# Optimization experiments

Measured on AMD Instinct MI355X. Metric: run time of the kernel, lower is better.

The kernel has to match this reference:

```python
import jax, jax.numpy as jnp
import numpy as np

MAX_VAL = 10000.0


def _erode(x, kernel):
    # x: (B, C, H, W); kernel: (kh, kw) flat structuring element (nonzero = active)
    kh, kw = kernel.shape
    oy, ox = kh // 2, kw // 2  # origin = center (rounding toward zero)
    padded = jnp.pad(
        x,
        ((0, 0), (0, 0), (oy, kh - oy - 1), (ox, kw - ox - 1)),
        mode="constant",
        constant_values=MAX_VAL,
    )
    # neighborhood bias: 0 where kernel != 0, -max_val where kernel == 0
    # output[p] = min_k ( padded[p + k] - neighborhood[k] )
    neigh = jnp.where(kernel == 0, -MAX_VAL, 0.0).astype(x.dtype)
    H, W = x.shape[-2], x.shape[-1]
    out = None
    for i in range(kh):  # small fixed k*k loop; no conv/im2col blow-up
        for j in range(kw):
            v = padded[:, :, i:i + H, j:j + W] - neigh[i, j]
            out = v if out is None else jnp.minimum(out, v)
    return out


def setup_inputs() -> dict:
    key = jax.random.key(0)
    x = jax.random.normal(key, (8, 8, 1024, 1024), dtype=jnp.float32)
    kernel = jnp.ones((3, 3), dtype=jnp.float32)
    return {"x": x, "kernel": kernel}


def reference(x, kernel):
    return _erode(x, kernel)
```

## Files before the change

kernel.cpp:

```cpp
#include <hip/hip_runtime.h>

#define MAXV 10000.0f

__global__ __launch_bounds__(256)
void erode3x3_kernel(const float* __restrict__ x,
                     const float* __restrict__ kern,
                     float* __restrict__ out,
                     int H, int W, int segs ) {
    long long idx = (long long)blockIdx.x * blockDim.x + threadIdx.x;
    int seg = (int)(idx % segs);
    int y   = (int)((idx / segs) % H);
    long long bc = idx / ((long long)segs * (long long)H);

    float nv[3][3];
#pragma unroll
    for (int i = 0; i < 3; ++i)
#pragma unroll
        for (int j = 0; j < 3; ++j)
            nv[i][j] = (kern[i * 3 + j] == 0.0f) ? -MAXV : 0.0f;

    const float* base = x + bc * (long long)H * (long long)W;
    const int x0 = seg * 4;

    float res0 = 3.4e38f, res1 = 3.4e38f, res2 = 3.4e38f, res3 = 3.4e38f;

#pragma unroll
    for (int i = 0; i < 3; ++i) {
        const int ry = y + i - 1;
        float v0, v1, v2, v3, v4, v5;
        if (ry >= 0 && ry < H) {
            const float* rp = base + (long long)ry * W + x0;
            const float4 b = *(const float4*)rp;
            v0 = (seg > 0)        ? rp[-1] : MAXV;
            v1 = b.x; v2 = b.y; v3 = b.z; v4 = b.w;
            v5 = (seg < segs - 1) ? rp[4]  : MAXV;
        } else {
            v0 = v1 = v2 = v3 = v4 = v5 = MAXV;
        }
        const float n0 = nv[i][0], n1 = nv[i][1], n2 = nv[i][2];
        res0 = fminf(res0, fminf(fminf(v0 - n0, v1 - n1), v2 - n2));
        res1 = fminf(res1, fminf(fminf(v1 - n0, v2 - n1), v3 - n2));
        res2 = fminf(res2, fminf(fminf(v2 - n0, v3 - n1), v4 - n2));
        res3 = fminf(res3, fminf(fminf(v3 - n0, v4 - n1), v5 - n2));
    }

    float4 o;
    o.x = res0; o.y = res1; o.z = res2; o.w = res3;
    *(float4*)(out + bc * (long long)H * W + (long long)y * W + x0) = o;
}

extern "C" void kernel_launch(void* const* d_in, const int* in_sizes, int n_in,
                              void* d_out, int out_size, void* d_ws, size_t ws_size,
                              hipStream_t stream) {
    const float* x    = (const float*)d_in[0];
    const float* kern = (const float*)d_in[1];
    float* out        = (float*)d_out;

    const int H = 1024, W = 1024;
    const int segs = W / 4;
    const long long total = (long long)out_size / 4;
    const int block = 256;
    const long long grid = (total + block - 1) / block;

    erode3x3_kernel<<<(dim3)(unsigned)grid, block, 0, stream>>>(
        x, kern, out, H, W, segs);
}
```

Before: 462.8 us.

## Process 16 output rows per thread with separable sliding-window min

Each thread now walks a vertical strip of 16 output rows and keeps three horizontal-min rows in registers, so each input row is loaded once per strip rather than three times. When every kernel entry is nonzero it takes a fast separable path that drops the bias subtraction and reuses the row minima. This cuts redundant global and L2 loads and ALU work. The cost is 16x fewer threads and a longer serial loop per thread, which could hurt latency hiding.

After: 439.0 us. 1.05x faster.

```diff
diff --git a/kernel.cpp b/kernel.cpp
--- a/kernel.cpp
+++ b/kernel.cpp
@@ -2,51 +2,105 @@
 
 #define MAXV 10000.0f
 
+__device__ __forceinline__ float min3f(float a, float b, float c) {
+    return fminf(fminf(a, b), c);
+}
+
+template <int R>
 __global__ __launch_bounds__(256)
-void erode3x3_kernel(const float* __restrict__ x,
-                     const float* __restrict__ kern,
-                     float* __restrict__ out,
-                     int H, int W, int segs ) {
-    long long idx = (long long)blockIdx.x * blockDim.x + threadIdx.x;
-    int seg = (int)(idx % segs);
-    int y   = (int)((idx / segs) % H);
-    long long bc = idx / ((long long)segs * (long long)H);
+void erode3x3_rows(const float* __restrict__ x,
+                   const float* __restrict__ kern,
+                   float* __restrict__ out,
+                   int H, int W, int segs, int ytiles) {
+    long long gid = (long long)blockIdx.x * blockDim.x + threadIdx.x;
+    int seg   = (int)(gid % segs);
+    int ytile = (int)((gid / segs) % ytiles);
+    long long bc = gid / ((long long)segs * ytiles);
 
     float nv[3][3];
+    bool all_active = true;
 #pragma unroll
     for (int i = 0; i < 3; ++i)
 #pragma unroll
-        for (int j = 0; j < 3; ++j)
-            nv[i][j] = (kern[i * 3 + j] == 0.0f) ? -MAXV : 0.0f;
+        for (int j = 0; j < 3; ++j) {
+            float kv = kern[i * 3 + j];
+            nv[i][j] = (kv == 0.0f) ? -MAXV : 0.0f;
+            all_active = all_active && (kv != 0.0f);
+        }
 
-    const float* base = x + bc * (long long)H * (long long)W;
+    const int y0 = ytile * R;
     const int x0 = seg * 4;
+    const float* base  = x   + bc * (long long)H * W;
+    float*       obase = out + bc * (long long)H * W;
 
-    float res0 = 3.4e38f, res1 = 3.4e38f, res2 = 3.4e38f, res3 = 3.4e38f;
-
+    if (all_active) {
+        float4 ha, hb, hc;
+        ha.x = ha.y = ha.z = ha.w = MAXV;
+        hb = ha; hc = ha;
 #pragma unroll
-    for (int i = 0; i < 3; ++i) {
-        const int ry = y + i - 1;
-        float v0, v1, v2, v3, v4, v5;
-        if (ry >= 0 && ry < H) {
-            const float* rp = base + (long long)ry * W + x0;
-            const float4 b = *(const float4*)rp;
-            v0 = (seg > 0)        ? rp[-1] : MAXV;
-            v1 = b.x; v2 = b.y; v3 = b.z; v4 = b.w;
-            v5 = (seg < segs - 1) ? rp[4]  : MAXV;
-        } else {
-            v0 = v1 = v2 = v3 = v4 = v5 = MAXV;
+        for (int r = 0; r < R + 2; ++r) {
+            const int ry = y0 - 1 + r;
+            float4 h;
+            if (ry >= 0 && ry < H) {
+                const float* rp = base + (long long)ry * W + x0;
+                const float4 b = *(const float4*)rp;
+                const float v0 = (seg > 0)        ? rp[-1] : MAXV;
+                const float v5 = (seg < segs - 1) ? rp[4]  : MAXV;
+                h.x = min3f(v0,  b.x, b.y);
+                h.y = min3f(b.x, b.y, b.z);
+                h.z = min3f(b.y, b.z, b.w);
+                h.w = min3f(b.z, b.w, v5);
+            } else {
+                h.x = h.y = h.z = h.w = MAXV;
+            }
+            ha = hb; hb = hc; hc = h;
+            if (r >= 2) {
+                float4 o;
+                o.x = min3f(ha.x, hb.x, hc.x);
+                o.y = min3f(ha.y, hb.y, hc.y);
+                o.z = min3f(ha.z, hb.z, hc.z);
+                o.w = min3f(ha.w, hb.w, hc.w);
+                *(float4*)(obase + (long long)(ry - 1) * W + x0) = o;
+            }
         }
-        const float n0 = nv[i][0], n1 = nv[i][1], n2 = nv[i][2];
-        res0 = fminf(res0, fminf(fminf(v0 - n0, v1 - n1), v2 - n2));
-        res1 = fminf(res1, fminf(fminf(v1 - n0, v2 - n1), v3 - n2));
-        res2 = fminf(res2, fminf(fminf(v2 - n0, v3 - n1), v4 - n2));
-        res3 = fminf(res3, fminf(fminf(v3 - n0, v4 - n1), v5 - n2));
+    } else {
+        float a0[6], a1[6], a2[6];
+#pragma unroll
+        for (int j = 0; j < 6; ++j) { a0[j] = a1[j] = a2[j] = MAXV; }
+#pragma unroll
+        for (int r = 0; r < R + 2; ++r) {
+            const int ry = y0 - 1 + r;
+            float cur[6];
+            if (ry >= 0 && ry < H) {
+                const float* rp = base + (long long)ry * W + x0;
+                const float4 b = *(const float4*)rp;
+                cur[0] = (seg > 0)        ? rp[-1] : MAXV;
+                cur[1] = b.x; cur[2] = b.y; cur[3] = b.z; cur[4] = b.w;
+                cur[5] = (seg < segs - 1) ? rp[4]  : MAXV;
+            } else {
+#pragma unroll
+                for (int j = 0; j < 6; ++j) cur[j] = MAXV;
+            }
+#pragma unroll
+            for (int j = 0; j < 6; ++j) { a0[j] = a1[j]; a1[j] = a2[j]; a2[j] = cur[j]; }
+            if (r >= 2) {
+                float o[4];
+#pragma unroll
+                for (int e = 0; e < 4; ++e) {
+                    float m = 3.4e38f;
+#pragma unroll
+                    for (int j = 0; j < 3; ++j) {
+                        m = fminf(m, a0[e + j] - nv[0][j]);
+                        m = fminf(m, a1[e + j] - nv[1][j]);
+                        m = fminf(m, a2[e + j] - nv[2][j]);
+                    }
+                    o[e] = m;
+                }
+                float4 ov; ov.x = o[0]; ov.y = o[1]; ov.z = o[2]; ov.w = o[3];
+                *(float4*)(obase + (long long)(ry - 1) * W + x0) = ov;
+            }
+        }
     }
-
-    float4 o;
-    o.x = res0; o.y = res1; o.z = res2; o.w = res3;
-    *(float4*)(out + bc * (long long)H * W + (long long)y * W + x0) = o;
 }
 
 extern "C" void kernel_launch(void* const* d_in, const int* in_sizes, int n_in,
@@ -57,11 +111,15 @@
     float* out        = (float*)d_out;
 
     const int H = 1024, W = 1024;
-    const int segs = W / 4;
-    const long long total = (long long)out_size / 4;
+    constexpr int R = 16;
+    const int segs   = W / 4;
+    const int ytiles = H / R;
+    const long long BC = (long long)out_size / ((long long)H * W);
+
+    const long long total = BC * (long long)ytiles * segs;
     const int block = 256;
     const long long grid = (total + block - 1) / block;
 
-    erode3x3_kernel<<<(dim3)(unsigned)grid, block, 0, stream>>>(
-        x, kern, out, H, W, segs);
+    erode3x3_rows<R><<<(dim3)(unsigned)grid, block, 0, stream>>>(
+        x, kern, out, H, W, segs, ytiles);
 }
```
